# Performance work log

Hardware: AMD Instinct MI355X
Metric: run time of the kernel (lower is better)

## Reference

```python
import jax, jax.numpy as jnp
import numpy as np

B, N_IN, N_OUT, NNZ, IN_C, OUT_C = 2, 50000, 12500, 500000, 256, 256


def setup_inputs() -> dict:
    key = jax.random.key(0)
    k1, k2, k3, k4, k5, k6 = jax.random.split(key, 6)
    x = jax.random.normal(k1, (B, N_IN, IN_C), dtype=jnp.float32)
    rows = jax.random.randint(k2, (NNZ,), 0, N_OUT, dtype=jnp.int32)
    cols = jax.random.randint(k3, (NNZ,), 0, N_IN, dtype=jnp.int32)
    vals = jax.random.uniform(k4, (NNZ,), dtype=jnp.float32)
    weight = jax.random.normal(k5, (IN_C, OUT_C), dtype=jnp.float32) / N_OUT
    bias = jax.random.normal(k6, (N_OUT, OUT_C), dtype=jnp.float32) / N_OUT
    return {"x": x, "rows": rows, "cols": cols, "vals": vals,
            "weight": weight, "bias": bias}


def reference(x, rows, cols, vals, weight, bias):
    # per-batch spmm: (A @ x_b) via gather + segment_sum, then dense projection.
    # Equivalent to the original block-diagonal torch.spmm over the batch.
    def spmm_one(xb):  # xb: [n_in, in_c]
        gathered = xb[cols] * vals[:, None]          # [nnz, in_c]
        return jax.ops.segment_sum(gathered, rows, num_segments=N_OUT)

    ax = jax.vmap(spmm_one)(x)                       # [B, n_out, in_c]
    return jnp.einsum('bni,io->bno', ax, weight) + bias
```

## Files before the change

kernel.cpp:

```cpp
#include <hip/hip_runtime.h>
#include <hip/hip_bf16.h>

typedef unsigned short u16;
typedef unsigned int   u32;
typedef __attribute__((ext_vector_type(8))) short bf16x8;
typedef __attribute__((ext_vector_type(4))) float f32x4;

constexpr int B_    = 2;
constexpr int N_IN  = 50000;
constexpr int N_OUT = 12500;
constexpr int NNZ   = 500000;
constexpr int C     = 256;
constexpr int M_TOT = B_ * N_OUT;

constexpr int QB = N_IN / 8;
constexpr int HB = (NNZ + 255) / 256;

__device__ __forceinline__ u16 f2b(float f) {
    __hip_bfloat16 h = __float2bfloat16(f);
    return *(u16*)&h;
}

__device__ __forceinline__ u32 pack4(float4 f, float inv) {
    u32 u0 = (u32)(int)(rintf(f.x * inv) + 128.f);
    u32 u1 = (u32)(int)(rintf(f.y * inv) + 128.f);
    u32 u2 = (u32)(int)(rintf(f.z * inv) + 128.f);
    u32 u3 = (u32)(int)(rintf(f.w * inv) + 128.f);
    return u0 | (u1 << 8) | (u2 << 16) | (u3 << 24);
}

__global__ __launch_bounds__(256) void quant_hist_k(const float* __restrict__ x,
                                                    u32* __restrict__ xq,
                                                    float* __restrict__ xs,
                                                    const int* __restrict__ rows,
                                                    int* __restrict__ counts) {
    int blk = blockIdx.x;
    int t   = threadIdx.x;
    if (blk < QB) {
        int wv  = t >> 6, l = t & 63;
        int rec = l >> 4;
        int j   = l & 15;
        int n   = blk * 8 + wv * 2 + (rec >> 1);
        int b   = rec & 1;
        const float4* px = (const float4*)(x + ((size_t)b * N_IN + n) * C + j * 16);
        float4 f0 = px[0], f1 = px[1], f2 = px[2], f3 = px[3];
        float m0 = fmaxf(fmaxf(fabsf(f0.x), fabsf(f0.y)), fmaxf(fabsf(f0.z), fabsf(f0.w)));
        float m1 = fmaxf(fmaxf(fabsf(f1.x), fabsf(f1.y)), fmaxf(fabsf(f1.z), fabsf(f1.w)));
        float m2 = fmaxf(fmaxf(fabsf(f2.x), fabsf(f2.y)), fmaxf(fabsf(f2.z), fabsf(f2.w)));
        float m3 = fmaxf(fmaxf(fabsf(f3.x), fabsf(f3.y)), fmaxf(fabsf(f3.z), fabsf(f3.w)));
        float m  = fmaxf(fmaxf(m0, m1), fmaxf(m2, m3));
#pragma unroll
        for (int off = 1; off < 16; off <<= 1)
            m = fmaxf(m, __shfl_xor(m, off, 64));
        float qstep = m * (1.f / 127.f);
        float inv   = 127.f / m;
        if (j == 0) xs[n * 2 + b] = qstep;
        uint4 pk;
        pk.x = pack4(f0, inv);
        pk.y = pack4(f1, inv);
        pk.z = pack4(f2, inv);
        pk.w = pack4(f3, inv);
        *(uint4*)(xq + (size_t)n * 128 + b * 64 + j * 4) = pk;
    } else {
        int i = (blk - QB) * 256 + t;
        if (i < NNZ) atomicAdd(&counts[rows[i]], 1);
    }
}

constexpr int CHUNK = (N_OUT + 255) / 256;
__global__ __launch_bounds__(256) void scan_tw_k(const int* __restrict__ counts,
                                                 int* __restrict__ start,
                                                 int* __restrict__ cursor,
                                                 const float* __restrict__ w,
                                                 u16* __restrict__ wt) {
    int tid = threadIdx.x;
    if (blockIdx.x > 0) {
        int n = blockIdx.x - 1;
        wt[(size_t)n * C + tid] = f2b(w[(size_t)tid * C + n]);
        return;
    }
    int base = tid * CHUNK;
    int s = 0;
    for (int j = 0; j < CHUNK; ++j) {
        int i = base + j;
        s += (i < N_OUT) ? counts[i] : 0;
    }
    int lane = tid & 63, wv = tid >> 6;
    int v = s;
#pragma unroll
    for (int off = 1; off < 64; off <<= 1) {
        int t2 = __shfl_up(v, off, 64);
        if (lane >= off) v += t2;
    }
    __shared__ int wsum[4];
    if (lane == 63) wsum[wv] = v;
    __syncthreads();
    int woff = 0;
    for (int ww = 0; ww < wv; ++ww) woff += wsum[ww];
    if (tid == 255) start[N_OUT] = woff + v;
    int run = woff + v - s;
    for (int j = 0; j < CHUNK; ++j) {
        int i = base + j;
        if (i < N_OUT) {
            start[i]  = run;
            cursor[i] = run;
            run += counts[i];
        }
    }
}

__global__ void scatter_k(const int* __restrict__ rows, const int* __restrict__ cols,
                          const float* __restrict__ vals, int* __restrict__ cursor,
                          int2* __restrict__ edges) {
    int i = blockIdx.x * blockDim.x + threadIdx.x;
    if (i < NNZ) {
        int r = rows[i];
        int p = atomicAdd(&cursor[r], 1);
        edges[p] = make_int2(cols[i], __float_as_int(vals[i]));
    }
}

__global__ __launch_bounds__(256) void spmm_q_k(const u32* __restrict__ xq,
                                                const float* __restrict__ xs,
                                                const int* __restrict__ start,
                                                const int2* __restrict__ edges,
                                                u32* __restrict__ ax) {
    int r    = blockIdx.x;
    int wv   = threadIdx.x >> 6;
    int lane = threadIdx.x & 63;
    int b    = lane >> 5;
    int g    = lane & 31;
    int loff = b * 64 + g * 2;

    int e0 = start[r], e1 = start[r + 1];
    float acc[8];
#pragma unroll
    for (int j = 0; j < 8; ++j) acc[j] = 0.f;
    float S = 0.f;

    auto body = [&](int2 d) {
        float vs = __int_as_float(d.y) * xs[d.x * 2 + b];
        uint2 q  = *(const uint2*)(xq + (size_t)d.x * 128 + loff);
        S += vs;
        acc[0] += vs * (float)( q.x        & 255u);
        acc[1] += vs * (float)((q.x >>  8) & 255u);
        acc[2] += vs * (float)((q.x >> 16) & 255u);
        acc[3] += vs * (float)( q.x >> 24        );
        acc[4] += vs * (float)( q.y        & 255u);
        acc[5] += vs * (float)((q.y >>  8) & 255u);
        acc[6] += vs * (float)((q.y >> 16) & 255u);
        acc[7] += vs * (float)( q.y >> 24        );
    };

    int e = e0 + wv;
    for (; e + 12 < e1; e += 16) {
        int2 d0 = edges[e], d1 = edges[e + 4], d2 = edges[e + 8], d3 = edges[e + 12];
        body(d0); body(d1); body(d2); body(d3);
    }
    for (; e < e1; e += 4) body(edges[e]);

    __shared__ float red[4][64][8];
#pragma unroll
    for (int j = 0; j < 8; ++j) red[wv][lane][j] = acc[j] - 128.f * S;
    __syncthreads();
    if (wv == 0) {
        float4 lo = *(float4*)&red[0][lane][0];
        float4 hi = *(float4*)&red[0][lane][4];
#pragma unroll
        for (int ww = 1; ww < 4; ++ww) {
            float4 l2 = *(float4*)&red[ww][lane][0];
            float4 h2 = *(float4*)&red[ww][lane][4];
            lo.x += l2.x; lo.y += l2.y; lo.z += l2.z; lo.w += l2.w;
            hi.x += h2.x; hi.y += h2.y; hi.z += h2.z; hi.w += h2.w;
        }
        uint4 pk;
        pk.x = (u32)f2b(lo.x) | ((u32)f2b(lo.y) << 16);
        pk.y = (u32)f2b(lo.z) | ((u32)f2b(lo.w) << 16);
        pk.z = (u32)f2b(hi.x) | ((u32)f2b(hi.y) << 16);
        pk.w = (u32)f2b(hi.z) | ((u32)f2b(hi.w) << 16);
        u32* axrow = ax + ((size_t)b * N_OUT + r) * (C / 2);
        *(uint4*)(axrow + g * 4) = pk;
    }
}

__global__ __launch_bounds__(256) void gemm_k(const u32* __restrict__ ax,
                                              const u16* __restrict__ wt,
                                              const float* __restrict__ bias,
                                              float* __restrict__ out) {
    int wave = threadIdx.x >> 6;
    int lane = threadIdx.x & 63;
    int quad = lane >> 4;
    int l15  = lane & 15;
    int m0   = blockIdx.x * 16;
    int n0   = wave * 64;

    int mrow = m0 + l15;
    int mr_c = mrow < M_TOT ? mrow : (M_TOT - 1);
    const u16* arow = (const u16*)(ax + (size_t)mr_c * (C / 2));

    f32x4 acc[4];
#pragma unroll
    for (int t = 0; t < 4; ++t) acc[t] = (f32x4){0.f, 0.f, 0.f, 0.f};

#pragma unroll
    for (int kt = 0; kt < 8; ++kt) {
        int k0 = kt * 32 + quad * 8;
        bf16x8 afrag = *(const bf16x8*)(arow + k0);
#pragma unroll
        for (int nt = 0; nt < 4; ++nt) {
            bf16x8 bfrag = *(const bf16x8*)(wt + (size_t)(n0 + nt * 16 + l15) * C + k0);
            acc[nt] = __builtin_amdgcn_mfma_f32_16x16x32_bf16(afrag, bfrag, acc[nt], 0, 0, 0);
        }
    }

#pragma unroll
    for (int nt = 0; nt < 4; ++nt) {
        int col = n0 + nt * 16 + l15;
#pragma unroll
        for (int reg = 0; reg < 4; ++reg) {
            int rg = m0 + quad * 4 + reg;
            if (rg < M_TOT) {
                int rloc = (rg >= N_OUT) ? rg - N_OUT : rg;
                out[(size_t)rg * C + col] = acc[nt][reg] + bias[(size_t)rloc * C + col];
            }
        }
    }
}

extern "C" void kernel_launch(void* const* d_in, const int* in_sizes, int n_in,
                              void* d_out, int out_size, void* d_ws, size_t ws_size,
                              hipStream_t stream) {
    const float* x      = (const float*)d_in[0];
    const int*   rows   = (const int*)d_in[1];
    const int*   cols   = (const int*)d_in[2];
    const float* vals   = (const float*)d_in[3];
    const float* weight = (const float*)d_in[4];
    const float* bias   = (const float*)d_in[5];
    float*       out    = (float*)d_out;

    char*  ws  = (char*)d_ws;
    size_t off = 0;
    auto alloc = [&](size_t bytes) -> void* {
        void* p = ws + off;
        off = (off + bytes + 255) & ~(size_t)255;
        return p;
    };
    int*   counts = (int*)  alloc((size_t)N_OUT * 4);
    int*   start  = (int*)  alloc((size_t)(N_OUT + 1) * 4);
    int*   cursor = (int*)  alloc((size_t)N_OUT * 4);
    int2*  edges  = (int2*) alloc((size_t)NNZ * 8);
    u32*   ax     = (u32*)  alloc((size_t)M_TOT * (C / 2) * 4);
    u16*   wt     = (u16*)  alloc((size_t)C * C * 2);
    u32*   xq     = (u32*)  alloc((size_t)N_IN * 128 * 4);
    float* xs     = (float*)alloc((size_t)N_IN * B_ * 4);
    if (off > ws_size) return;

    hipMemsetAsync(counts, 0, (size_t)N_OUT * 4, stream);

    quant_hist_k<<<QB + HB, 256, 0, stream>>>(x, xq, xs, rows, counts);
    scan_tw_k   <<<1 + C, 256, 0, stream>>>(counts, start, cursor, weight, wt);
    scatter_k   <<<HB, 256, 0, stream>>>(rows, cols, vals, cursor, edges);
    spmm_q_k    <<<N_OUT, 256, 0, stream>>>(xq, xs, start, edges, ax);
    gemm_k      <<<(M_TOT + 15) / 16, 256, 0, stream>>>(ax, wt, bias, out);
}
```

Before: 339.7 us.

## Replace global atomic CSR build with block-local LDS histograms and scatter

Replaces the global-atomic histogram and scatter used to build the row-sorted edge list with a two-level scheme. 128 blocks each build an LDS histogram over a contiguous chunk of edges, a per-bin prefix over blocks gives each block its offsets, and the scatter then uses LDS atomics. The memset and the fused quant/histogram kernel are split into separate launches, and the temporary partial counts reuse the ax buffer. This removes contended global atomics but adds two launches and only 128 blocks for the histogram and scatter phases, so those phases may be underparallel.

```diff
diff --git a/kernel.cpp b/kernel.cpp
--- a/kernel.cpp
+++ b/kernel.cpp
@@ -13,8 +13,9 @@
 constexpr int C     = 256;
 constexpr int M_TOT = B_ * N_OUT;
 
-constexpr int QB = N_IN / 8;
-constexpr int HB = (NNZ + 255) / 256;
+constexpr int QB   = N_IN / 8;
+constexpr int NB_H = 128;
+constexpr int EPB  = (NNZ + NB_H - 1) / NB_H;
 
 __device__ __forceinline__ u16 f2b(float f) {
     __hip_bfloat16 h = __float2bfloat16(f);
@@ -29,48 +30,69 @@
     return u0 | (u1 << 8) | (u2 << 16) | (u3 << 24);
 }
 
-__global__ __launch_bounds__(256) void quant_hist_k(const float* __restrict__ x,
-                                                    u32* __restrict__ xq,
-                                                    float* __restrict__ xs,
-                                                    const int* __restrict__ rows,
-                                                    int* __restrict__ counts) {
+__global__ __launch_bounds__(256) void quant_k(const float* __restrict__ x,
+                                               u32* __restrict__ xq,
+                                               float* __restrict__ xs) {
     int blk = blockIdx.x;
     int t   = threadIdx.x;
-    if (blk < QB) {
-        int wv  = t >> 6, l = t & 63;
-        int rec = l >> 4;
-        int j   = l & 15;
-        int n   = blk * 8 + wv * 2 + (rec >> 1);
-        int b   = rec & 1;
-        const float4* px = (const float4*)(x + ((size_t)b * N_IN + n) * C + j * 16);
-        float4 f0 = px[0], f1 = px[1], f2 = px[2], f3 = px[3];
-        float m0 = fmaxf(fmaxf(fabsf(f0.x), fabsf(f0.y)), fmaxf(fabsf(f0.z), fabsf(f0.w)));
-        float m1 = fmaxf(fmaxf(fabsf(f1.x), fabsf(f1.y)), fmaxf(fabsf(f1.z), fabsf(f1.w)));
-        float m2 = fmaxf(fmaxf(fabsf(f2.x), fabsf(f2.y)), fmaxf(fabsf(f2.z), fabsf(f2.w)));
-        float m3 = fmaxf(fmaxf(fabsf(f3.x), fabsf(f3.y)), fmaxf(fabsf(f3.z), fabsf(f3.w)));
-        float m  = fmaxf(fmaxf(m0, m1), fmaxf(m2, m3));
-#pragma unroll
-        for (int off = 1; off < 16; off <<= 1)
-            m = fmaxf(m, __shfl_xor(m, off, 64));
-        float qstep = m * (1.f / 127.f);
-        float inv   = 127.f / m;
-        if (j == 0) xs[n * 2 + b] = qstep;
-        uint4 pk;
-        pk.x = pack4(f0, inv);
-        pk.y = pack4(f1, inv);
-        pk.z = pack4(f2, inv);
-        pk.w = pack4(f3, inv);
-        *(uint4*)(xq + (size_t)n * 128 + b * 64 + j * 4) = pk;
-    } else {
-        int i = (blk - QB) * 256 + t;
-        if (i < NNZ) atomicAdd(&counts[rows[i]], 1);
-    }
+    int wv  = t >> 6, l = t & 63;
+    int rec = l >> 4;
+    int j   = l & 15;
+    int n   = blk * 8 + wv * 2 + (rec >> 1);
+    int b   = rec & 1;
+    const float4* px = (const float4*)(x + ((size_t)b * N_IN + n) * C + j * 16);
+    float4 f0 = px[0], f1 = px[1], f2 = px[2], f3 = px[3];
+    float m0 = fmaxf(fmaxf(fabsf(f0.x), fabsf(f0.y)), fmaxf(fabsf(f0.z), fabsf(f0.w)));
+    float m1 = fmaxf(fmaxf(fabsf(f1.x), fabsf(f1.y)), fmaxf(fabsf(f1.z), fabsf(f1.w)));
+    float m2 = fmaxf(fmaxf(fabsf(f2.x), fabsf(f2.y)), fmaxf(fabsf(f2.z), fabsf(f2.w)));
+    float m3 = fmaxf(fmaxf(fabsf(f3.x), fabsf(f3.y)), fmaxf(fabsf(f3.z), fabsf(f3.w)));
+    float m  = fmaxf(fmaxf(m0, m1), fmaxf(m2, m3));
+#pragma unroll
+    for (int off = 1; off < 16; off <<= 1)
+        m = fmaxf(m, __shfl_xor(m, off, 64));
+    float qstep = m * (1.f / 127.f);
+    float inv   = 127.f / m;
+    if (j == 0) xs[n * 2 + b] = qstep;
+    uint4 pk;
+    pk.x = pack4(f0, inv);
+    pk.y = pack4(f1, inv);
+    pk.z = pack4(f2, inv);
+    pk.w = pack4(f3, inv);
+    *(uint4*)(xq + (size_t)n * 128 + b * 64 + j * 4) = pk;
+}
+
+__global__ __launch_bounds__(256) void hist_k(const int* __restrict__ rows,
+                                              u16* __restrict__ partial) {
+    __shared__ u32 lc[N_OUT];
+    int t = threadIdx.x, blk = blockIdx.x;
+    for (int i = t; i < N_OUT; i += 256) lc[i] = 0;
+    __syncthreads();
+    int base = blk * EPB;
+    int end  = base + EPB < NNZ ? base + EPB : NNZ;
+    for (int i = base + t; i < end; i += 256)
+        atomicAdd(&lc[rows[i]], 1u);
+    __syncthreads();
+    for (int i = t; i < N_OUT; i += 256)
+        partial[(size_t)blk * N_OUT + i] = (u16)lc[i];
+}
+
+__global__ __launch_bounds__(256) void binprefix_k(const u16* __restrict__ partial,
+                                                   u16* __restrict__ bp,
+                                                   int* __restrict__ counts) {
+    int bin = blockIdx.x * 256 + threadIdx.x;
+    if (bin >= N_OUT) return;
+    u32 run = 0;
+    for (int b = 0; b < NB_H; ++b) {
+        u32 c = partial[(size_t)b * N_OUT + bin];
+        bp[(size_t)b * N_OUT + bin] = (u16)run;
+        run += c;
+    }
+    counts[bin] = (int)run;
 }
 
 constexpr int CHUNK = (N_OUT + 255) / 256;
 __global__ __launch_bounds__(256) void scan_tw_k(const int* __restrict__ counts,
                                                  int* __restrict__ start,
-                                                 int* __restrict__ cursor,
                                                  const float* __restrict__ w,
                                                  u16* __restrict__ wt) {
     int tid = threadIdx.x;
@@ -102,20 +124,28 @@
     for (int j = 0; j < CHUNK; ++j) {
         int i = base + j;
         if (i < N_OUT) {
-            start[i]  = run;
-            cursor[i] = run;
+            start[i] = run;
             run += counts[i];
         }
     }
 }
 
-__global__ void scatter_k(const int* __restrict__ rows, const int* __restrict__ cols,
-                          const float* __restrict__ vals, int* __restrict__ cursor,
-                          int2* __restrict__ edges) {
-    int i = blockIdx.x * blockDim.x + threadIdx.x;
-    if (i < NNZ) {
+__global__ __launch_bounds__(256) void scatter_k(const int* __restrict__ rows,
+                                                 const int* __restrict__ cols,
+                                                 const float* __restrict__ vals,
+                                                 const int* __restrict__ start,
+                                                 const u16* __restrict__ bp,
+                                                 int2* __restrict__ edges) {
+    __shared__ u32 lc[N_OUT];
+    int t = threadIdx.x, blk = blockIdx.x;
+    for (int i = t; i < N_OUT; i += 256)
+        lc[i] = (u32)start[i] + (u32)bp[(size_t)blk * N_OUT + i];
+    __syncthreads();
+    int base = blk * EPB;
+    int end  = base + EPB < NNZ ? base + EPB : NNZ;
+    for (int i = base + t; i < end; i += 256) {
         int r = rows[i];
-        int p = atomicAdd(&cursor[r], 1);
+        u32 p = atomicAdd(&lc[r], 1u);
         edges[p] = make_int2(cols[i], __float_as_int(vals[i]));
     }
 }
@@ -247,7 +277,6 @@
     };
     int*   counts = (int*)  alloc((size_t)N_OUT * 4);
     int*   start  = (int*)  alloc((size_t)(N_OUT + 1) * 4);
-    int*   cursor = (int*)  alloc((size_t)N_OUT * 4);
     int2*  edges  = (int2*) alloc((size_t)NNZ * 8);
     u32*   ax     = (u32*)  alloc((size_t)M_TOT * (C / 2) * 4);
     u16*   wt     = (u16*)  alloc((size_t)C * C * 2);
@@ -255,11 +284,14 @@
     float* xs     = (float*)alloc((size_t)N_IN * B_ * 4);
     if (off > ws_size) return;
 
-    hipMemsetAsync(counts, 0, (size_t)N_OUT * 4, stream);
-
-    quant_hist_k<<<QB + HB, 256, 0, stream>>>(x, xq, xs, rows, counts);
-    scan_tw_k   <<<1 + C, 256, 0, stream>>>(counts, start, cursor, weight, wt);
-    scatter_k   <<<HB, 256, 0, stream>>>(rows, cols, vals, cursor, edges);
-    spmm_q_k    <<<N_OUT, 256, 0, stream>>>(xq, xs, start, edges, ax);
-    gemm_k      <<<(M_TOT + 15) / 16, 256, 0, stream>>>(ax, wt, bias, out);
-}
+    u16* partial = (u16*)ax;
+    u16* bp      = partial + (size_t)NB_H * N_OUT;
+
+    quant_k    <<<QB, 256, 0, stream>>>(x, xq, xs);
+    hist_k     <<<NB_H, 256, 0, stream>>>(rows, partial);
+    binprefix_k<<<(N_OUT + 255) / 256, 256, 0, stream>>>(partial, bp, counts);
+    scan_tw_k  <<<1 + C, 256, 0, stream>>>(counts, start, weight, wt);
+    scatter_k  <<<NB_H, 256, 0, stream>>>(rows, cols, vals, start, bp, edges);
+    spmm_q_k   <<<N_OUT, 256, 0, stream>>>(xq, xs, start, edges, ax);
+    gemm_k     <<<(M_TOT + 15) / 16, 256, 0, stream>>>(ax, wt, bias, out);
+}
```

Result: faster. 326.0 us (-4.0%).
